# Optimization experiments

Hardware: AMD Instinct MI355X
Metric: run time of the kernel (lower is better)

Reference implementation:

```python
import jax, jax.numpy as jnp
import numpy as np

B, C, H, W = 4, 64, 128, 128
F_FEA, D, NH = 6, 512, 128  # n_features, latent_vector_size, SPADE hidden


def conv3x3(x, w, b):
    y = jax.lax.conv_general_dilated(
        x, w, window_strides=(1, 1), padding=((1, 1), (1, 1)),
        dimension_numbers=('NCHW', 'OIHW', 'NCHW'))
    return y + b[None, :, None, None]


def setup_inputs() -> dict:
    key = jax.random.key(0)
    ks = jax.random.split(key, 16)
    s = 0.02
    x = jax.random.normal(ks[0], (B, C, H, W), jnp.float32)
    labels = jax.random.randint(ks[1], (B, H, W), 0, F_FEA)
    segmap = jnp.transpose(jax.nn.one_hot(labels, F_FEA, dtype=jnp.float32), (0, 3, 1, 2))
    mask = jax.random.uniform(ks[2], (B, 3, H, W), dtype=jnp.float32)
    codes_vector = jax.random.normal(ks[3], (B, F_FEA, D), jnp.float32)
    noise = jax.random.normal(ks[4], (B, W, H, 1), jnp.float32)
    return {
        'x': x, 'segmap': segmap, 'mask': mask, 'codes_vector': codes_vector, 'noise': noise,
        'noise_var': jax.random.normal(ks[5], (C,), jnp.float32) * s,
        'fc_w': jax.random.normal(ks[6], (F_FEA, D, D), jnp.float32) * s,
        'fc_b': jnp.zeros((F_FEA, D), jnp.float32),
        'conv_gamma_w': jax.random.normal(ks[7], (C, D, 3, 3), jnp.float32) * s,
        'conv_gamma_b': jnp.zeros((C,), jnp.float32),
        'conv_beta_w': jax.random.normal(ks[8], (C, D, 3, 3), jnp.float32) * s,
        'conv_beta_b': jnp.zeros((C,), jnp.float32),
        'sp_shared_w': jax.random.normal(ks[9], (NH, 3, 3, 3), jnp.float32) * s,
        'sp_shared_b': jnp.zeros((NH,), jnp.float32),
        'sp_gamma_w': jax.random.normal(ks[10], (C, NH, 3, 3), jnp.float32) * s,
        'sp_gamma_b': jnp.zeros((C,), jnp.float32),
        'sp_beta_w': jax.random.normal(ks[11], (C, NH, 3, 3), jnp.float32) * s,
        'sp_beta_b': jnp.zeros((C,), jnp.float32),
        'blending_gamma': jnp.zeros((1,), jnp.float32),
        'blending_beta': jnp.zeros((1,), jnp.float32),
    }


def reference(x, segmap, mask, codes_vector, noise, noise_var, fc_w, fc_b,
              conv_gamma_w, conv_gamma_b, conv_beta_w, conv_beta_b,
              sp_shared_w, sp_shared_b, sp_gamma_w, sp_gamma_b,
              sp_beta_w, sp_beta_b, blending_gamma, blending_beta):
    # additive per-channel noise: randn(B,W,H,1)*noise_var -> transpose(1,3) -> (B,C,H,W)
    added_noise = jnp.transpose(noise * noise_var, (0, 3, 2, 1))
    xn = x + added_noise
    # InstanceNorm2d (affine=False, eps=1e-5): normalize per sample, per channel over H,W
    mu = xn.mean(axis=(2, 3), keepdims=True)
    var = xn.var(axis=(2, 3), keepdims=True)
    x_norm = (xn - mu) * jax.lax.rsqrt(var + 1e-5)

    # per-facial-feature Linear(512,512) + ReLU, batched over B and features: [B,F,D]
    middle_mu = jax.nn.relu(jnp.einsum('bfd,fod->bfo', codes_vector, fc_w) + fc_b)

    # region embedding: broadcast each feature's code over its segmap region
    # (masked_scatter_ semantics: later features overwrite earlier ones on overlap)
    n_fea = fc_w.shape[0]
    lat = fc_w.shape[1]
    middle_avg = jnp.zeros((x.shape[0], lat, x.shape[2], x.shape[3]), x.dtype)
    for j in range(n_fea):
        m = (segmap[:, j] != 0)[:, None]  # [B,1,H,W]
        middle_avg = jnp.where(m, middle_mu[:, j, :, None, None], middle_avg)

    gamma_avg = conv3x3(middle_avg, conv_gamma_w, conv_gamma_b)
    beta_avg = conv3x3(middle_avg, conv_beta_w, conv_beta_b)

    # SPADE on mask (already at x's spatial size; nearest-interp is identity)
    actv = jax.nn.relu(conv3x3(mask, sp_shared_w, sp_shared_b))
    gamma_spade = conv3x3(actv, sp_gamma_w, sp_gamma_b)
    beta_spade = conv3x3(actv, sp_beta_w, sp_beta_b)

    ga = jax.nn.sigmoid(blending_gamma)[0]
    ba = jax.nn.sigmoid(blending_beta)[0]
    gamma_final = ga * gamma_avg + (1 - ga) * gamma_spade
    beta_final = ba * beta_avg + (1 - ba) * beta_spade
    return x_norm * (1 + gamma_final) + beta_final
```

## Files before the change

kernel.cpp:

```cpp
#include <hip/hip_runtime.h>
#include <hip/hip_bf16.h>
#include <math.h>

#define BB 4
#define CC 64
#define HH 128
#define WW 128
#define FF 6
#define DD 512
#define NHH 128
#define HWSZ (HH*WW)

typedef unsigned short u16;
typedef __attribute__((ext_vector_type(4))) unsigned short u16x4;
typedef __attribute__((ext_vector_type(8))) short short8;
typedef __attribute__((ext_vector_type(4))) float f32x4;

__device__ inline float b2f(u16 u){
  union { unsigned int i; float f; } v; v.i = ((unsigned int)u) << 16; return v.f;
}
__device__ inline u16 f2b(float f){
  union { float f; unsigned int i; } v; v.f = f;
  unsigned int r = v.i + 0x7fffu + ((v.i >> 16) & 1u);
  return (u16)(r >> 16);
}

__global__ void k_labels(const float* __restrict__ seg, int* __restrict__ lab){
  int i = blockIdx.x * 256 + threadIdx.x;
  int b = i >> 14; int hw = i & 16383;
  int l = -1;
  #pragma unroll
  for (int j = 0; j < FF; j++){
    float v = seg[(b*FF + j)*HWSZ + hw];
    if (v != 0.f) l = j;
  }
  lab[i] = l;
}

__global__ void k_nzT(const float* __restrict__ noise, float* __restrict__ nzT){
  __shared__ float tile[32][33];
  int blk = blockIdx.x;
  int b = blk >> 4, t = blk & 15;
  int ti = t & 3, tj = t >> 2;
  int h0 = ti*32, w0 = tj*32;
  int tx = threadIdx.x & 31, ty = threadIdx.x >> 5;
  #pragma unroll
  for (int k = 0; k < 4; k++){
    int r = ty + 8*k;
    tile[r][tx] = noise[b*HWSZ + (w0+r)*128 + h0 + tx];
  }
  __syncthreads();
  #pragma unroll
  for (int k = 0; k < 4; k++){
    int r = ty + 8*k;
    nzT[b*HWSZ + (h0+r)*128 + w0 + tx] = tile[tx][r];
  }
}

__global__ void k_stats(const float* __restrict__ x, const float* __restrict__ nzT,
                        const float* __restrict__ nvar, float* __restrict__ mu,
                        float* __restrict__ rs){
  int bc = blockIdx.x; int b = bc >> 6; int c = bc & 63;
  float nv = nvar[c];
  const float4* xp = (const float4*)(x + (size_t)bc * HWSZ);
  const float4* np = (const float4*)(nzT + (size_t)b * HWSZ);
  float s = 0.f, ss = 0.f;
  for (int i = threadIdx.x; i < HWSZ/4; i += 256){
    float4 xv = xp[i], nn = np[i];
    float v0 = xv.x + nn.x*nv, v1 = xv.y + nn.y*nv;
    float v2 = xv.z + nn.z*nv, v3 = xv.w + nn.w*nv;
    s += v0+v1+v2+v3;
    ss += v0*v0 + v1*v1 + v2*v2 + v3*v3;
  }
  #pragma unroll
  for (int off = 32; off; off >>= 1){
    s  += __shfl_down(s, off);
    ss += __shfl_down(ss, off);
  }
  __shared__ float wsum[4], wss[4];
  int wi = threadIdx.x >> 6, lane = threadIdx.x & 63;
  if (lane == 0){ wsum[wi] = s; wss[wi] = ss; }
  __syncthreads();
  if (threadIdx.x == 0){
    float S = wsum[0]+wsum[1]+wsum[2]+wsum[3];
    float SS = wss[0]+wss[1]+wss[2]+wss[3];
    float m = S / (float)HWSZ;
    float var = SS / (float)HWSZ - m*m;
    mu[bc] = m; rs[bc] = rsqrtf(var + 1e-5f);
  }
}

__global__ __launch_bounds__(256) void k_mm(const float* __restrict__ codes,
                     const float* __restrict__ fcw,
                     const float* __restrict__ fcb, float* __restrict__ mm){
  int blk = blockIdx.x;
  int og = blk & 7, bf = blk >> 3; int f = bf % FF;
  __shared__ float sc[DD];
  int tid = threadIdx.x;
  for (int i = tid; i < DD; i += 256) sc[i] = codes[bf*DD + i];
  __syncthreads();
  int wi = tid >> 6, lane = tid & 63;
  for (int oo = 0; oo < 16; oo += 2){
    int o1 = og*64 + wi*16 + oo, o2 = o1 + 1;
    const float* w1 = fcw + ((size_t)(f*DD + o1)) * DD;
    const float* w2 = w1 + DD;
    float a1 = 0.f, a2 = 0.f;
    #pragma unroll
    for (int k = 0; k < 8; k++){
      int d = lane + k*64;
      float sv = sc[d];
      a1 += sv * w1[d];
      a2 += sv * w2[d];
    }
    #pragma unroll
    for (int off = 32; off; off >>= 1){
      a1 += __shfl_down(a1, off);
      a2 += __shfl_down(a2, off);
    }
    if (lane == 0){
      mm[bf*DD + o1] = fmaxf(a1 + fcb[f*DD + o1], 0.f);
      mm[bf*DD + o2] = fmaxf(a2 + fcb[f*DD + o2], 0.f);
    }
  }
}

__global__ __launch_bounds__(576) void k_p(const float* __restrict__ mm,
                    const float* __restrict__ wg,
                    const float* __restrict__ wb, float* __restrict__ Pg,
                    float* __restrict__ Pb){
  int blk = blockIdx.x;
  int cg = blk & 7, bf = blk >> 3;
  __shared__ float smm[DD];
  __shared__ float pg[8][72], pb[8][72];
  int tid = threadIdx.x;
  for (int i = tid; i < DD; i += 576) smm[i] = mm[bf*DD + i];
  __syncthreads();
  int ds = tid / 72, rem = tid % 72;
  int c8 = rem / 9, t = rem % 9;
  int c = cg*8 + c8;
  const float* wgp = wg + (size_t)c * DD * 9 + t;
  const float* wbp = wb + (size_t)c * DD * 9 + t;
  float ag = 0.f, ab = 0.f;
  int d0 = ds * 64;
  #pragma unroll 4
  for (int d = d0; d < d0 + 64; d++){
    float m = smm[d];
    ag += m * wgp[d*9];
    ab += m * wbp[d*9];
  }
  pg[ds][rem] = ag; pb[ds][rem] = ab;
  __syncthreads();
  if (tid < 72){
    float sg = 0.f, sb = 0.f;
    #pragma unroll
    for (int k = 0; k < 8; k++){ sg += pg[k][tid]; sb += pb[k][tid]; }
    int cc = cg*8 + tid/9, tt = tid%9;
    Pg[bf*576 + tt*64 + cc] = sg;
    Pb[bf*576 + tt*64 + cc] = sb;
  }
}

__global__ void k_actv(const float* __restrict__ mask, const float* __restrict__ w,
                       const float* __restrict__ bias, u16* __restrict__ actv){
  int bh = blockIdx.x;
  int b = bh >> 7; int h = bh & 127;
  int tw = threadIdx.x;
  float mreg[3][3][3];
  #pragma unroll
  for (int ci = 0; ci < 3; ci++)
    #pragma unroll
    for (int r = 0; r < 3; r++){
      int hh = h - 1 + r;
      #pragma unroll
      for (int dx = 0; dx < 3; dx++){
        int ww2 = tw - 1 + dx;
        mreg[ci][r][dx] = (hh >= 0 && hh < HH && ww2 >= 0 && ww2 < WW)
                          ? mask[((b*3 + ci)*HH + hh)*WW + ww2] : 0.f;
      }
    }
  __shared__ float sw[NHH*27];
  for (int i = threadIdx.x; i < NHH*27; i += 128) sw[i] = w[i];
  __shared__ float sb[NHH];
  sb[threadIdx.x] = bias[threadIdx.x];
  __syncthreads();
  u16* outp = actv + ((size_t)bh * WW + tw) * NHH;
  for (int n0 = 0; n0 < NHH; n0 += 4){
    u16x4 pkt;
    #pragma unroll
    for (int j = 0; j < 4; j++){
      int n = n0 + j;
      float acc = sb[n];
      const float* wn = &sw[n*27];
      #pragma unroll
      for (int ci = 0; ci < 3; ci++)
        #pragma unroll
        for (int r = 0; r < 3; r++)
          #pragma unroll
          for (int dx = 0; dx < 3; dx++)
            acc += mreg[ci][r][dx] * wn[ci*9 + r*3 + dx];
      pkt[j] = f2b(fmaxf(acc, 0.f));
    }
    *(u16x4*)(outp + n0) = pkt;
  }
}

__global__ void k_bw(const float* __restrict__ sgw, const float* __restrict__ sbw,
                     u16* __restrict__ BwT){
  int idx = blockIdx.x*256 + threadIdx.x;
  int j = idx / 1152, k = idx - j*1152;
  int tap = k >> 7, n = k & 127;
  float v = (j < 64) ? sgw[(j*NHH + n)*9 + tap] : sbw[((j-64)*NHH + n)*9 + tap];
  BwT[idx] = f2b(v);
}

__global__ __launch_bounds__(256, 2) void k_spade(const u16* __restrict__ actv,
    const u16* __restrict__ BwT, const int* __restrict__ lab,
    const float* __restrict__ Pgf, const float* __restrict__ Pbf,
    const float* __restrict__ x, const float* __restrict__ nzT,
    const float* __restrict__ nvar, const float* __restrict__ mu,
    const float* __restrict__ rs,
    const float* __restrict__ cgb, const float* __restrict__ cbb,
    const float* __restrict__ sgb, const float* __restrict__ sbb,
    const float* __restrict__ blg, const float* __restrict__ blb,
    float* __restrict__ out)
{
  int bh = blockIdx.x; int b = bh >> 7; int h = bh & 127;
  __shared__ __align__(16) u16 Ub[18432];
  __shared__ float sPg[64*57];
  __shared__ float sPb[64*57];
  __shared__ int sLab[390];
  u16* Ash = Ub;
  u16* Bsh = Ub + 9216;

  int tid = threadIdx.x;
  int wid = tid >> 6, lane = tid & 63;
  int wr = wid >> 1, wc = wid & 1;
  int l15 = lane & 15, lhi = lane >> 4;

  for (int i = tid; i < 3456; i += 256){
    int lt = i >> 6, c = i & 63;
    sPg[c*57 + lt] = Pgf[b*3456 + i];
    sPb[c*57 + lt] = Pbf[b*3456 + i];
  }
  for (int i = tid; i < 390; i += 256){
    int r = i / 130, ww2 = i % 130;
    int hh = h - 1 + r, w2 = ww2 - 1;
    sLab[i] = (hh >= 0 && hh < HH && w2 >= 0 && w2 < WW)
              ? lab[b*HWSZ + hh*WW + w2] : -1;
  }

  f32x4 acc[4][4];
  #pragma unroll
  for (int mi = 0; mi < 4; mi++)
    #pragma unroll
    for (int ni = 0; ni < 4; ni++) acc[mi][ni] = 0.f;

  const u16* ab = actv + (size_t)b * HWSZ * NHH;

  for (int kt = 0; kt < 18; kt++){
    int tap = kt >> 1, n0 = (kt & 1) << 6;
    int r = tap / 3, dx = tap - r*3;
    int h2 = h - 1 + r;
    bool hok = (h2 >= 0) && (h2 < HH);
    for (int i = tid; i < 1024; i += 256){
      int pix = i >> 3, cp = i & 7;
      int w2 = pix - 1 + dx;
      short8 v = 0;
      if (hok && w2 >= 0 && w2 < WW)
        v = *(const short8*)(ab + (((size_t)h2*WW + w2)*NHH + n0 + cp*8));
      *(short8*)&Ash[pix*72 + cp*8] = v;
    }
    for (int i = tid; i < 1024; i += 256){
      int n = i >> 3, cp = i & 7;
      *(short8*)&Bsh[n*72 + cp*8] = *(const short8*)(BwT + (size_t)n*1152 + kt*64 + cp*8);
    }
    __syncthreads();
    short8 af[4][2], bfr[2][4];
    #pragma unroll
    for (int mi = 0; mi < 4; mi++)
      #pragma unroll
      for (int ks = 0; ks < 2; ks++)
        af[mi][ks] = *(const short8*)&Ash[(wr*64 + mi*16 + l15)*72 + ks*32 + lhi*8];
    #pragma unroll
    for (int ks = 0; ks < 2; ks++)
      #pragma unroll
      for (int ni = 0; ni < 4; ni++)
        bfr[ks][ni] = *(const short8*)&Bsh[(wc*64 + ni*16 + l15)*72 + ks*32 + lhi*8];
    #pragma unroll
    for (int mi = 0; mi < 4; mi++)
      #pragma unroll
      for (int ni = 0; ni < 4; ni++)
        #pragma unroll
        for (int ks = 0; ks < 2; ks++)
          acc[mi][ni] = __builtin_amdgcn_mfma_f32_16x16x32_bf16(
              af[mi][ks], bfr[ks][ni], acc[mi][ni], 0, 0, 0);
    __syncthreads();
  }

  u16* spGB = Ub;
  #pragma unroll
  for (int mi = 0; mi < 4; mi++){
    int w0 = wr*64 + mi*16 + lhi*4;
    #pragma unroll
    for (int ni = 0; ni < 4; ni++){
      int j = wc*64 + ni*16 + l15;
      u16x4 pkt;
      #pragma unroll
      for (int q = 0; q < 4; q++) pkt[q] = f2b(acc[mi][ni][q]);
      *(u16x4*)&spGB[j*132 + w0] = pkt;
    }
  }
  __syncthreads();

  float sga = 1.f / (1.f + expf(-blg[0]));
  float sba = 1.f / (1.f + expf(-blb[0]));
  int w = tid & 127, chalf = tid >> 7;
  float nzv = nzT[b*HWSZ + h*128 + w];
  for (int it = 0; it < 32; it++){
    int c = it*2 + chalf;
    int bc = b*CC + c;
    float g  = b2f(spGB[c*132 + w])        + sgb[c];
    float bt = b2f(spGB[(64 + c)*132 + w]) + sbb[c];
    float gA = cgb[c], bA = cbb[c];
    #pragma unroll
    for (int t = 0; t < 9; t++){
      int r = t/3, dx = t - r*3;
      int l = sLab[r*130 + w + dx];
      if (l >= 0){
        gA += sPg[c*57 + l*9 + t];
        bA += sPb[c*57 + l*9 + t];
      }
    }
    float gf  = sga*gA + (1.f - sga)*g;
    float bfv = sba*bA + (1.f - sba)*bt;
    size_t idx = (size_t)bc*HWSZ + h*128 + w;
    float xn = x[idx] + nzv * nvar[c];
    float xnorm = (xn - mu[bc]) * rs[bc];
    out[idx] = xnorm * (1.f + gf) + bfv;
  }
}

extern "C" void kernel_launch(void* const* d_in, const int* in_sizes, int n_in,
                              void* d_out, int out_size, void* d_ws, size_t ws_size,
                              hipStream_t stream){
  const float* x     = (const float*)d_in[0];
  const float* seg   = (const float*)d_in[1];
  const float* mask  = (const float*)d_in[2];
  const float* codes = (const float*)d_in[3];
  const float* noise = (const float*)d_in[4];
  const float* nvar  = (const float*)d_in[5];
  const float* fcw   = (const float*)d_in[6];
  const float* fcb   = (const float*)d_in[7];
  const float* cgw   = (const float*)d_in[8];
  const float* cgb   = (const float*)d_in[9];
  const float* cbw   = (const float*)d_in[10];
  const float* cbb   = (const float*)d_in[11];
  const float* ssw   = (const float*)d_in[12];
  const float* ssb   = (const float*)d_in[13];
  const float* sgw   = (const float*)d_in[14];
  const float* sgb   = (const float*)d_in[15];
  const float* sbw   = (const float*)d_in[16];
  const float* sbb   = (const float*)d_in[17];
  const float* blg   = (const float*)d_in[18];
  const float* blb   = (const float*)d_in[19];
  float* out = (float*)d_out;

  char* ws = (char*)d_ws;
  int*   lab  = (int*)ws;
  float* mu   = (float*)(ws + 262144);
  float* rs   = (float*)(ws + 263168);
  float* mm   = (float*)(ws + 264192);
  float* Pg   = (float*)(ws + 313344);
  float* Pb   = (float*)(ws + 368640);
  u16*   BwT  = (u16*)(ws + 423936);
  float* nzT  = (float*)(ws + 718848);
  u16*   actv = (u16*)(ws + 980992);

  k_labels<<<dim3((BB*HWSZ)/256), dim3(256), 0, stream>>>(seg, lab);
  k_nzT   <<<dim3(BB*16),        dim3(256), 0, stream>>>(noise, nzT);
  k_stats <<<dim3(BB*CC),        dim3(256), 0, stream>>>(x, nzT, nvar, mu, rs);
  k_mm    <<<dim3(BB*FF*8),      dim3(256), 0, stream>>>(codes, fcw, fcb, mm);
  k_p     <<<dim3(BB*FF*8),      dim3(576), 0, stream>>>(mm, cgw, cbw, Pg, Pb);
  k_bw    <<<dim3(576),          dim3(256), 0, stream>>>(sgw, sbw, BwT);
  k_actv  <<<dim3(BB*HH),        dim3(128), 0, stream>>>(mask, ssw, ssb, actv);
  k_spade <<<dim3(BB*HH),        dim3(256), 0, stream>>>(
      actv, BwT, lab, Pg, Pb, x, nzT, nvar, mu, rs,
      cgb, cbb, sgb, sbb, blg, blb, out);
}
```

Measured before the change: 265.1 us.

## Double-buffer SPADE conv tiles, merge prep kernels, and restructure P projection with bf16 weights

The main SPADE MFMA loop now prefetches the next K-tile of activations and weights into registers while the current tile is consumed, and writes it into a second LDS A buffer. This hides global-load latency behind the matrix ops. The label and noise-transpose kernels are merged into one launch, and so are the two weight-conversion kernels. The conv-weight projection (k_p) now works on a transposed bf16 copy of the weights using wave-wide reductions. The per-label P tables are stored in LDS as packed bf16 pairs, and neighbor labels are hoisted into registers. In exchange, the conv_gamma/beta weights are converted to bf16 on every call, which adds extra weight traffic, and the P values lose precision.

```diff
diff --git a/kernel.cpp b/kernel.cpp
--- a/kernel.cpp
+++ b/kernel.cpp
@@ -25,35 +25,37 @@
   return (u16)(r >> 16);
 }
 
-__global__ void k_labels(const float* __restrict__ seg, int* __restrict__ lab){
-  int i = blockIdx.x * 256 + threadIdx.x;
-  int b = i >> 14; int hw = i & 16383;
-  int l = -1;
-  #pragma unroll
-  for (int j = 0; j < FF; j++){
-    float v = seg[(b*FF + j)*HWSZ + hw];
-    if (v != 0.f) l = j;
-  }
-  lab[i] = l;
-}
-
-__global__ void k_nzT(const float* __restrict__ noise, float* __restrict__ nzT){
-  __shared__ float tile[32][33];
+__global__ void k_prep(const float* __restrict__ seg, const float* __restrict__ noise,
+                       int* __restrict__ lab, float* __restrict__ nzT){
   int blk = blockIdx.x;
-  int b = blk >> 4, t = blk & 15;
-  int ti = t & 3, tj = t >> 2;
-  int h0 = ti*32, w0 = tj*32;
-  int tx = threadIdx.x & 31, ty = threadIdx.x >> 5;
-  #pragma unroll
-  for (int k = 0; k < 4; k++){
-    int r = ty + 8*k;
-    tile[r][tx] = noise[b*HWSZ + (w0+r)*128 + h0 + tx];
-  }
-  __syncthreads();
-  #pragma unroll
-  for (int k = 0; k < 4; k++){
-    int r = ty + 8*k;
-    nzT[b*HWSZ + (h0+r)*128 + w0 + tx] = tile[tx][r];
+  if (blk < 256){
+    int i = blk * 256 + threadIdx.x;
+    int b = i >> 14; int hw = i & 16383;
+    int l = -1;
+    #pragma unroll
+    for (int j = 0; j < FF; j++){
+      float v = seg[(b*FF + j)*HWSZ + hw];
+      if (v != 0.f) l = j;
+    }
+    lab[i] = l;
+  } else {
+    __shared__ float tile[32][33];
+    int t2 = blk - 256;
+    int b = t2 >> 4, t = t2 & 15;
+    int ti = t & 3, tj = t >> 2;
+    int h0 = ti*32, w0 = tj*32;
+    int tx = threadIdx.x & 31, ty = threadIdx.x >> 5;
+    #pragma unroll
+    for (int k = 0; k < 4; k++){
+      int r = ty + 8*k;
+      tile[r][tx] = noise[b*HWSZ + (w0+r)*128 + h0 + tx];
+    }
+    __syncthreads();
+    #pragma unroll
+    for (int k = 0; k < 4; k++){
+      int r = ty + 8*k;
+      nzT[b*HWSZ + (h0+r)*128 + w0 + tx] = tile[tx][r];
+    }
   }
 }
 
@@ -124,39 +126,48 @@
   }
 }
 
-__global__ __launch_bounds__(576) void k_p(const float* __restrict__ mm,
-                    const float* __restrict__ wg,
-                    const float* __restrict__ wb, float* __restrict__ Pg,
-                    float* __restrict__ Pb){
+__global__ void k_bwp(const float* __restrict__ sgw, const float* __restrict__ sbw,
+                      const float* __restrict__ cgw, const float* __restrict__ cbw,
+                      u16* __restrict__ BwT, u16* __restrict__ WtP){
   int blk = blockIdx.x;
-  int cg = blk & 7, bf = blk >> 3;
-  __shared__ float smm[DD];
-  __shared__ float pg[8][72], pb[8][72];
-  int tid = threadIdx.x;
-  for (int i = tid; i < DD; i += 576) smm[i] = mm[bf*DD + i];
-  __syncthreads();
-  int ds = tid / 72, rem = tid % 72;
-  int c8 = rem / 9, t = rem % 9;
-  int c = cg*8 + c8;
-  const float* wgp = wg + (size_t)c * DD * 9 + t;
-  const float* wbp = wb + (size_t)c * DD * 9 + t;
-  float ag = 0.f, ab = 0.f;
-  int d0 = ds * 64;
-  #pragma unroll 4
-  for (int d = d0; d < d0 + 64; d++){
-    float m = smm[d];
-    ag += m * wgp[d*9];
-    ab += m * wbp[d*9];
-  }
-  pg[ds][rem] = ag; pb[ds][rem] = ab;
-  __syncthreads();
-  if (tid < 72){
-    float sg = 0.f, sb = 0.f;
-    #pragma unroll
-    for (int k = 0; k < 8; k++){ sg += pg[k][tid]; sb += pb[k][tid]; }
-    int cc = cg*8 + tid/9, tt = tid%9;
-    Pg[bf*576 + tt*64 + cc] = sg;
-    Pb[bf*576 + tt*64 + cc] = sb;
+  if (blk < 576){
+    int idx = blk*256 + threadIdx.x;
+    int j = idx / 1152, k = idx - j*1152;
+    int tap = k >> 7, n = k & 127;
+    float v = (j < 64) ? sgw[(j*NHH + n)*9 + tap] : sbw[((j-64)*NHH + n)*9 + tap];
+    BwT[idx] = f2b(v);
+  } else {
+    int idx = (blk - 576)*256 + threadIdx.x;
+    int mat = idx / 294912; int rr = idx - mat*294912;
+    int tc = rr >> 9, d = rr & 511;
+    int t = tc >> 6, c = tc & 63;
+    const float* src = mat ? cbw : cgw;
+    WtP[idx] = f2b(src[(c*DD + d)*9 + t]);
+  }
+}
+
+__global__ __launch_bounds__(256) void k_p(const float* __restrict__ mm,
+                    const u16* __restrict__ WtP,
+                    float* __restrict__ Pg, float* __restrict__ Pb){
+  int blk = blockIdx.x;
+  int q = blk % 6, bf = blk / 6;
+  int wid = threadIdx.x >> 6, lane = threadIdx.x & 63;
+  const float4* mp = (const float4*)(mm + bf*DD + lane*8);
+  float4 m0 = mp[0], m1 = mp[1];
+  float mv[8] = {m0.x, m0.y, m0.z, m0.w, m1.x, m1.y, m1.z, m1.w};
+  int t0 = q*192 + wid*48;
+  for (int j = 0; j < 48; j++){
+    int tt = t0 + j;
+    int mat = tt / 576, tc = tt - mat*576;
+    short8 wv = *(const short8*)(WtP + ((size_t)mat*576 + tc)*DD + lane*8);
+    float s = 0.f;
+    #pragma unroll
+    for (int k = 0; k < 8; k++) s += b2f((u16)wv[k]) * mv[k];
+    #pragma unroll
+    for (int off = 32; off; off >>= 1) s += __shfl_down(s, off);
+    if (lane == 0){
+      if (mat) Pb[bf*576 + tc] = s; else Pg[bf*576 + tc] = s;
+    }
   }
 }
 
@@ -204,14 +215,30 @@
   }
 }
 
-__global__ void k_bw(const float* __restrict__ sgw, const float* __restrict__ sbw,
-                     u16* __restrict__ BwT){
-  int idx = blockIdx.x*256 + threadIdx.x;
-  int j = idx / 1152, k = idx - j*1152;
-  int tap = k >> 7, n = k & 127;
-  float v = (j < 64) ? sgw[(j*NHH + n)*9 + tap] : sbw[((j-64)*NHH + n)*9 + tap];
-  BwT[idx] = f2b(v);
-}
+#define LOADT(kt_) { \
+  int tap = (kt_) >> 1, n0 = ((kt_) & 1) << 6; \
+  int rr = tap/3, dx = tap - rr*3; \
+  int h2 = h - 1 + rr; bool hok = (h2>=0) && (h2<HH); \
+  _Pragma("unroll") \
+  for (int it = 0; it < 4; it++){ \
+    int i = it*256 + tid; \
+    int pix = i >> 3, cp = i & 7; \
+    int w2 = pix - 1 + dx; \
+    short8 v = 0; \
+    if (hok && w2 >= 0 && w2 < WW) \
+      v = *(const short8*)(ab + (((size_t)h2*WW + w2)*NHH + n0 + cp*8)); \
+    Ar[it] = v; \
+    Br[it] = *(const short8*)(BwT + (size_t)pix*1152 + (kt_)*64 + cp*8); \
+  } }
+
+#define WRITET(buf_) { \
+  _Pragma("unroll") \
+  for (int it = 0; it < 4; it++){ \
+    int i = it*256 + tid; \
+    int pix = i >> 3, cp = i & 7; \
+    *(short8*)&Ash[buf_][pix*72 + cp*8] = Ar[it]; \
+    *(short8*)&Bsh[pix*72 + cp*8] = Br[it]; \
+  } }
 
 __global__ __launch_bounds__(256, 2) void k_spade(const u16* __restrict__ actv,
     const u16* __restrict__ BwT, const int* __restrict__ lab,
@@ -225,12 +252,10 @@
     float* __restrict__ out)
 {
   int bh = blockIdx.x; int b = bh >> 7; int h = bh & 127;
-  __shared__ __align__(16) u16 Ub[18432];
-  __shared__ float sPg[64*57];
-  __shared__ float sPb[64*57];
+  __shared__ __align__(16) u16 Ash[2][128*72];
+  __shared__ __align__(16) u16 Bsh[128*72];
+  __shared__ u16 sP[64*57*2];
   __shared__ int sLab[390];
-  u16* Ash = Ub;
-  u16* Bsh = Ub + 9216;
 
   int tid = threadIdx.x;
   int wid = tid >> 6, lane = tid & 63;
@@ -239,8 +264,10 @@
 
   for (int i = tid; i < 3456; i += 256){
     int lt = i >> 6, c = i & 63;
-    sPg[c*57 + lt] = Pgf[b*3456 + i];
-    sPb[c*57 + lt] = Pbf[b*3456 + i];
+    int f = lt / 9, t = lt - f*9;
+    int gidx = (b*FF + f)*576 + t*64 + c;
+    sP[(c*57 + lt)*2 + 0] = f2b(Pgf[gidx]);
+    sP[(c*57 + lt)*2 + 1] = f2b(Pbf[gidx]);
   }
   for (int i = tid; i < 390; i += 256){
     int r = i / 130, ww2 = i % 130;
@@ -256,31 +283,22 @@
     for (int ni = 0; ni < 4; ni++) acc[mi][ni] = 0.f;
 
   const u16* ab = actv + (size_t)b * HWSZ * NHH;
-
+  short8 Ar[4], Br[4];
+
+  LOADT(0)
+  WRITET(0)
+  __syncthreads();
+
+  int cur = 0;
   for (int kt = 0; kt < 18; kt++){
-    int tap = kt >> 1, n0 = (kt & 1) << 6;
-    int r = tap / 3, dx = tap - r*3;
-    int h2 = h - 1 + r;
-    bool hok = (h2 >= 0) && (h2 < HH);
-    for (int i = tid; i < 1024; i += 256){
-      int pix = i >> 3, cp = i & 7;
-      int w2 = pix - 1 + dx;
-      short8 v = 0;
-      if (hok && w2 >= 0 && w2 < WW)
-        v = *(const short8*)(ab + (((size_t)h2*WW + w2)*NHH + n0 + cp*8));
-      *(short8*)&Ash[pix*72 + cp*8] = v;
-    }
-    for (int i = tid; i < 1024; i += 256){
-      int n = i >> 3, cp = i & 7;
-      *(short8*)&Bsh[n*72 + cp*8] = *(const short8*)(BwT + (size_t)n*1152 + kt*64 + cp*8);
-    }
-    __syncthreads();
+    if (kt < 17) LOADT(kt+1)
+    __builtin_amdgcn_sched_barrier(0);
     short8 af[4][2], bfr[2][4];
     #pragma unroll
     for (int mi = 0; mi < 4; mi++)
       #pragma unroll
       for (int ks = 0; ks < 2; ks++)
-        af[mi][ks] = *(const short8*)&Ash[(wr*64 + mi*16 + l15)*72 + ks*32 + lhi*8];
+        af[mi][ks] = *(const short8*)&Ash[cur][(wr*64 + mi*16 + l15)*72 + ks*32 + lhi*8];
     #pragma unroll
     for (int ks = 0; ks < 2; ks++)
       #pragma unroll
@@ -295,9 +313,12 @@
           acc[mi][ni] = __builtin_amdgcn_mfma_f32_16x16x32_bf16(
               af[mi][ks], bfr[ks][ni], acc[mi][ni], 0, 0, 0);
     __syncthreads();
-  }
-
-  u16* spGB = Ub;
+    if (kt < 17) WRITET(cur^1)
+    __syncthreads();
+    cur ^= 1;
+  }
+
+  u16* spGB = &Ash[0][0];
   #pragma unroll
   for (int mi = 0; mi < 4; mi++){
     int w0 = wr*64 + mi*16 + lhi*4;
@@ -316,6 +337,12 @@
   float sba = 1.f / (1.f + expf(-blb[0]));
   int w = tid & 127, chalf = tid >> 7;
   float nzv = nzT[b*HWSZ + h*128 + w];
+  int lt9[9];
+  #pragma unroll
+  for (int t = 0; t < 9; t++){
+    int r = t/3, dx = t - r*3;
+    lt9[t] = sLab[r*130 + w + dx];
+  }
   for (int it = 0; it < 32; it++){
     int c = it*2 + chalf;
     int bc = b*CC + c;
@@ -324,11 +351,11 @@
     float gA = cgb[c], bA = cbb[c];
     #pragma unroll
     for (int t = 0; t < 9; t++){
-      int r = t/3, dx = t - r*3;
-      int l = sLab[r*130 + w + dx];
+      int l = lt9[t];
       if (l >= 0){
-        gA += sPg[c*57 + l*9 + t];
-        bA += sPb[c*57 + l*9 + t];
+        unsigned pr = *(const unsigned*)&sP[(c*57 + l*9 + t)*2];
+        gA += b2f((u16)(pr & 0xffffu));
+        bA += b2f((u16)(pr >> 16));
       }
     }
     float gf  = sga*gA + (1.f - sga)*g;
@@ -374,14 +401,14 @@
   float* Pb   = (float*)(ws + 368640);
   u16*   BwT  = (u16*)(ws + 423936);
   float* nzT  = (float*)(ws + 718848);
-  u16*   actv = (u16*)(ws + 980992);
-
-  k_labels<<<dim3((BB*HWSZ)/256), dim3(256), 0, stream>>>(seg, lab);
-  k_nzT   <<<dim3(BB*16),        dim3(256), 0, stream>>>(noise, nzT);
+  u16*   WtP  = (u16*)(ws + 980992);
+  u16*   actv = (u16*)(ws + 2160640);
+
+  k_prep  <<<dim3(320),          dim3(256), 0, stream>>>(seg, noise, lab, nzT);
   k_stats <<<dim3(BB*CC),        dim3(256), 0, stream>>>(x, nzT, nvar, mu, rs);
   k_mm    <<<dim3(BB*FF*8),      dim3(256), 0, stream>>>(codes, fcw, fcb, mm);
-  k_p     <<<dim3(BB*FF*8),      dim3(576), 0, stream>>>(mm, cgw, cbw, Pg, Pb);
-  k_bw    <<<dim3(576),          dim3(256), 0, stream>>>(sgw, sbw, BwT);
+  k_bwp   <<<dim3(2880),         dim3(256), 0, stream>>>(sgw, sbw, cgw, cbw, BwT, WtP);
+  k_p     <<<dim3(BB*FF*6),      dim3(256), 0, stream>>>(mm, WtP, Pg, Pb);
   k_actv  <<<dim3(BB*HH),        dim3(128), 0, stream>>>(mask, ssw, ssb, actv);
   k_spade <<<dim3(BB*HH),        dim3(256), 0, stream>>>(
       actv, BwT, lab, Pg, Pb, x, nzT, nvar, mu, rs,
```

Result: faster. 258.1 us (-2.7%).
